# Performance work log

Hardware: AMD Instinct MI355X
Metric: run time of the kernel (lower is better)

Reference implementation:

```python
import jax, jax.numpy as jnp
import numpy as np

B, L, D = 8, 2048, 1024
NH = 16            # n_head
HD = D // NH       # 64; attention is (HD x HD) per token in this module


def setup_inputs() -> dict:
    key = jax.random.key(0)
    ks = jax.random.split(key, 5)
    s = 0.02  # init scale for weights
    return {
        "x": jax.random.normal(ks[0], (B, L, D), jnp.float32),
        "Wq": jax.random.normal(ks[1], (D, D), jnp.float32) * s,
        "bq": jnp.zeros((D,), jnp.float32),
        "Wk": jax.random.normal(ks[2], (D, D), jnp.float32) * s,
        "bk": jnp.zeros((D,), jnp.float32),
        "Wv": jax.random.normal(ks[3], (D, D), jnp.float32) * s,
        "bv": jnp.zeros((D,), jnp.float32),
        "Wo": jax.random.normal(ks[4], (D, D), jnp.float32) * s,
        "bo": jnp.zeros((D,), jnp.float32),
    }


def reference(x, Wq, bq, Wk, bk, Wv, bv, Wo, bo):
    b, l, d = x.shape
    # QKV projections
    q = (x @ Wq + bq).reshape(b, l, HD, NH)
    k = (x @ Wk + bk).reshape(b, l, HD, NH)
    v = (x @ Wv + bv).reshape(b, l, HD, NH)
    # NOTE: module reshapes to (b, l, head_dim, n_head), so scores are
    # per-token (HD, HD) with the NH axis contracted; norm = sqrt(NH).
    norm = jnp.sqrt(jnp.asarray(NH, x.dtype))
    attn = jnp.einsum('blij,blkj->blik', q, k) / norm  # (b, l, HD, HD)
    attn = attn + 1e-06
    # mask = tril of the VALUES; jnp.where uses nonzero-as-True semantics.
    mask = jnp.tril(attn)
    attn = jnp.where(mask, attn, -jnp.inf)
    probs = jax.nn.softmax(attn, axis=-1)
    y = jnp.einsum('blik,blkj->blij', probs, v).reshape(b, l, d)
    return y @ Wo + bo
```

## Files before the change

kernel.cpp:

```cpp
#include <hip/hip_runtime.h>
#include <hip/hip_bf16.h>
#include <stdint.h>

typedef unsigned short u16;

#define Bdim 8
#define Ldim 2048
#define Ddim 1024
#define NH 16
#define HD 64
#define MTOK (Bdim*Ldim)

#define BM 128
#define BN 128
#define BK 32

typedef __bf16 bf16x8 __attribute__((ext_vector_type(8)));
typedef float  f32x4  __attribute__((ext_vector_type(4)));
typedef float  f32x16 __attribute__((ext_vector_type(16)));

#define AS1 __attribute__((address_space(1)))
#define AS3 __attribute__((address_space(3)))

__device__ __forceinline__ void gload_lds16(const void* g, void* l) {
  __builtin_amdgcn_global_load_lds((const AS1 void*)g, (AS3 void*)l, 16, 0, 0);
}

__device__ __forceinline__ u16 f2bf(float f) {
  uint32_t u = __builtin_bit_cast(uint32_t, f);
  u += 0x7fffu + ((u >> 16) & 1u);
  return (u16)(u >> 16);
}
__device__ __forceinline__ uint32_t pkpair(float lo, float hi) {
  return (uint32_t)f2bf(lo) | ((uint32_t)f2bf(hi) << 16);
}

__global__ __launch_bounds__(256) void conv_f32_bf16(const float* __restrict__ in,
                                                     u16* __restrict__ out, int n4) {
  int i = blockIdx.x * 256 + threadIdx.x;
  if (i < n4) {
    float4 v = ((const float4*)in)[i];
    uint32_t w0 = (uint32_t)f2bf(v.x) | ((uint32_t)f2bf(v.y) << 16);
    uint32_t w1 = (uint32_t)f2bf(v.z) | ((uint32_t)f2bf(v.w) << 16);
    ((uint2*)out)[i] = make_uint2(w0, w1);
  }
}

__global__ __launch_bounds__(256) void conv_transpose_w(const float* __restrict__ W,
                                                        u16* __restrict__ Wt) {
  __shared__ float t[32][33];
  int tx = threadIdx.x & 31, ty = threadIdx.x >> 5;
  int k0 = blockIdx.x * 32, n0 = blockIdx.y * 32;
  #pragma unroll
  for (int i = 0; i < 32; i += 8)
    t[ty + i][tx] = W[(size_t)(k0 + ty + i) * Ddim + n0 + tx];
  __syncthreads();
  #pragma unroll
  for (int i = 0; i < 32; i += 8)
    Wt[(size_t)(n0 + ty + i) * Ddim + k0 + tx] = f2bf(t[tx][ty + i]);
}

template <int FUSED>
__global__ __launch_bounds__(256) void gemm_bt(const u16* __restrict__ A,
                                               const u16* __restrict__ Bt,
                                               const float* __restrict__ b0p,
                                               const float* __restrict__ b1p,
                                               const float* __restrict__ b2p,
                                               void* __restrict__ o0,
                                               void* __restrict__ o1,
                                               void* __restrict__ o2) {
  constexpr int K = 1024;
  __shared__ alignas(16) unsigned char pool[34816];
  u16* As = (u16*)pool;
  u16* Bs = As + 4096;
  const int tid = threadIdx.x;
  const int wid = tid >> 6, lane = tid & 63;
  const int bid = blockIdx.x;
  const int xcd = bid & 7, idx = bid >> 3;
  const int mt = (xcd << 4) | (idx & 15);
  const int nt = idx >> 4;
  const int m0 = mt * BM;
  const int n0g = nt * BN;
  const int wr = wid >> 1, wc = wid & 1;
  const int fr = lane & 15, fh = lane >> 4;

  f32x4 acc[4][4] = {};

  for (int k0 = 0; k0 < K; k0 += BK) {
    #pragma unroll
    for (int c = 0; c < 2; ++c) {
      int e = c * 2048 + wid * 512 + lane * 8;
      int r = e >> 5, col = e & 31;
      gload_lds16(A  + (size_t)(m0  + r) * K + (k0 + col), As + c * 2048 + wid * 512);
      gload_lds16(Bt + (size_t)(n0g + r) * K + (k0 + col), Bs + c * 2048 + wid * 512);
    }
    __syncthreads();

    bf16x8 af[4], bfr[4];
    #pragma unroll
    for (int m = 0; m < 4; ++m)
      af[m] = *(const bf16x8*)(As + (wr * 64 + m * 16 + fr) * BK + fh * 8);
    #pragma unroll
    for (int n = 0; n < 4; ++n)
      bfr[n] = *(const bf16x8*)(Bs + (wc * 64 + n * 16 + fr) * BK + fh * 8);
    #pragma unroll
    for (int m = 0; m < 4; ++m)
      #pragma unroll
      for (int n = 0; n < 4; ++n)
        acc[m][n] = __builtin_amdgcn_mfma_f32_16x16x32_bf16(af[m], bfr[n], acc[m][n], 0, 0, 0);
    __syncthreads();
  }

  if (FUSED) {
    const int which = nt >> 3;
    const int n0l = (nt & 7) * BN;
    const float* bias = which == 0 ? b0p : which == 1 ? b1p : b2p;
    u16* Out = (u16*)(which == 0 ? o0 : which == 1 ? o1 : o2);

    u16* Ct = (u16*)pool;
    #pragma unroll
    for (int n = 0; n < 4; ++n) {
      int col = wc * 64 + n * 16 + fr;
      float bvv = bias[n0l + col];
      #pragma unroll
      for (int m = 0; m < 4; ++m)
        #pragma unroll
        for (int r = 0; r < 4; ++r) {
          int row = wr * 64 + m * 16 + fh * 4 + r;
          Ct[row * 136 + col] = f2bf(acc[m][n][r] + bvv);
        }
    }
    __syncthreads();
    if (which != 2) {
      #pragma unroll
      for (int it = 0; it < 8; ++it) {
        int q = it * 256 + tid, r = q >> 4, cc = q & 15;
        uint4 v = *(const uint4*)(Ct + r * 136 + cc * 8);
        *(uint4*)(Out + (size_t)(m0 + r) * Ddim + n0l + cc * 8) = v;
      }
    } else {
      #pragma unroll
      for (int it = 0; it < 8; ++it) {
        int q = it * 256 + tid, r = q >> 4, i = q & 15;
        u16 tmp[8];
        #pragma unroll
        for (int j = 0; j < 8; ++j) tmp[j] = Ct[r * 136 + i + 16 * j];
        *(uint4*)(Out + (size_t)(m0 + r) * Ddim + i * 64 + (n0l >> 4)) = *(uint4*)tmp;
      }
    }
  } else {
    float* Cf = (float*)pool;
    float* Out = (float*)o0;
    #pragma unroll
    for (int h = 0; h < 2; ++h) {
      if (wc == h) {
        #pragma unroll
        for (int n = 0; n < 4; ++n) {
          int col = n * 16 + fr;
          float bvv = b0p[n0g + h * 64 + col];
          #pragma unroll
          for (int m = 0; m < 4; ++m)
            #pragma unroll
            for (int r = 0; r < 4; ++r) {
              int row = wr * 64 + m * 16 + fh * 4 + r;
              Cf[row * 68 + col] = acc[m][n][r] + bvv;
            }
        }
      }
      __syncthreads();
      #pragma unroll
      for (int it = 0; it < 8; ++it) {
        int q = it * 256 + tid, r = q >> 4, cc = q & 15;
        float4 v = *(const float4*)(Cf + r * 68 + cc * 4);
        *(float4*)(Out + (size_t)(m0 + r) * Ddim + n0g + h * 64 + cc * 4) = v;
      }
      __syncthreads();
    }
  }
}

__global__ __launch_bounds__(256) void attn_mfma(const u16* __restrict__ Q,
                                                 const u16* __restrict__ Kb,
                                                 const u16* __restrict__ Vt,
                                                 u16* __restrict__ Y) {
  const int wid = threadIdx.x >> 6, lane = threadIdx.x & 63;
  const int tok = blockIdx.x * 4 + wid;
  const size_t base = (size_t)tok * Ddim;
  const int hi = lane >> 5, c31 = lane & 31;

  const bf16x8 kf0 = *(const bf16x8*)(Kb + base + (size_t)c31 * NH + hi * 8);
  const bf16x8 kf1 = *(const bf16x8*)(Kb + base + (size_t)(32 + c31) * NH + hi * 8);
  const bf16x8 qf0 = *(const bf16x8*)(Q  + base + (size_t)c31 * NH + hi * 8);
  const bf16x8 qf1 = *(const bf16x8*)(Q  + base + (size_t)(32 + c31) * NH + hi * 8);
  bf16x8 bv[4];
  #pragma unroll
  for (int c = 0; c < 4; ++c)
    bv[c] = *(const bf16x8*)(Vt + base + (size_t)(lane & 15) * HD + c * 16 + hi * 8);

  const f32x16 z = {};
  f32x16 s00 = __builtin_amdgcn_mfma_f32_32x32x16_bf16(kf0, qf0, z, 0, 0, 0);
  f32x16 s01 = __builtin_amdgcn_mfma_f32_32x32x16_bf16(kf0, qf1, z, 0, 0, 0);
  f32x16 s11 = __builtin_amdgcn_mfma_f32_32x32x16_bf16(kf1, qf1, z, 0, 0, 0);

  float a[16], b0[16], b1[16];
  float mA = -3e38f, mB = -3e38f;
  #pragma unroll
  for (int r = 0; r < 16; ++r) {
    const int kl = (r & 3) + 8 * (r >> 2) + 4 * hi;
    const bool keep = kl <= c31;
    float v00 = fmaf(s00[r], 0.25f, 1e-6f);
    float v01 = fmaf(s01[r], 0.25f, 1e-6f);
    float v11 = fmaf(s11[r], 0.25f, 1e-6f);
    a[r]  = keep ? v00 : -3e38f;
    b0[r] = v01;
    b1[r] = keep ? v11 : -3e38f;
    mA = fmaxf(mA, a[r]);
    mB = fmaxf(mB, fmaxf(b0[r], b1[r]));
  }
  mA = fmaxf(mA, __shfl_xor(mA, 32, 64));
  mB = fmaxf(mB, __shfl_xor(mB, 32, 64));
  float sA = 0.f, sB = 0.f;
  #pragma unroll
  for (int r = 0; r < 16; ++r) {
    a[r]  = __expf(a[r]  - mA);  sA += a[r];
    b0[r] = __expf(b0[r] - mB);
    b1[r] = __expf(b1[r] - mB);  sB += b0[r] + b1[r];
  }
  sA += __shfl_xor(sA, 32, 64);
  sB += __shfl_xor(sB, 32, 64);
  const float iA = __builtin_amdgcn_rcpf(sA);
  const float iB = __builtin_amdgcn_rcpf(sB);

  uint32_t pA[4][2], pB0[4][2], pB1[4][2];
  #pragma unroll
  for (int m = 0; m < 4; ++m)
    #pragma unroll
    for (int t = 0; t < 2; ++t) {
      pA [m][t] = pkpair(a [4*m+2*t] * iA, a [4*m+2*t+1] * iA);
      pB0[m][t] = pkpair(b0[4*m+2*t] * iB, b0[4*m+2*t+1] * iB);
      pB1[m][t] = pkpair(b1[4*m+2*t] * iB, b1[4*m+2*t+1] * iB);
    }

#define AFRAG(dst, src, cp) do {                                              \
    uint32_t k0_ = hi ? src[2*(cp)+1][0] : src[2*(cp)][0];                    \
    uint32_t k1_ = hi ? src[2*(cp)+1][1] : src[2*(cp)][1];                    \
    uint32_t s0_ = hi ? src[2*(cp)][0]   : src[2*(cp)+1][0];                  \
    uint32_t s1_ = hi ? src[2*(cp)][1]   : src[2*(cp)+1][1];                  \
    uint32_t r0_ = (uint32_t)__shfl_xor((int)s0_, 32, 64);                    \
    uint32_t r1_ = (uint32_t)__shfl_xor((int)s1_, 32, 64);                    \
    union { uint32_t w[4]; bf16x8 v; } u_;                                    \
    u_.w[0] = hi ? r0_ : k0_;  u_.w[1] = hi ? r1_ : k1_;                      \
    u_.w[2] = hi ? k0_ : r0_;  u_.w[3] = hi ? k1_ : r1_;                      \
    dst = u_.v;                                                               \
  } while (0)

  f32x16 y0 = {}, y1 = {};
  bf16x8 af;
  AFRAG(af, pA, 0);  y0 = __builtin_amdgcn_mfma_f32_32x32x16_bf16(af, bv[0], y0, 0, 0, 0);
  AFRAG(af, pA, 1);  y0 = __builtin_amdgcn_mfma_f32_32x32x16_bf16(af, bv[1], y0, 0, 0, 0);
  AFRAG(af, pB0, 0); y1 = __builtin_amdgcn_mfma_f32_32x32x16_bf16(af, bv[0], y1, 0, 0, 0);
  AFRAG(af, pB0, 1); y1 = __builtin_amdgcn_mfma_f32_32x32x16_bf16(af, bv[1], y1, 0, 0, 0);
  AFRAG(af, pB1, 0); y1 = __builtin_amdgcn_mfma_f32_32x32x16_bf16(af, bv[2], y1, 0, 0, 0);
  AFRAG(af, pB1, 1); y1 = __builtin_amdgcn_mfma_f32_32x32x16_bf16(af, bv[3], y1, 0, 0, 0);
#undef AFRAG

  if (c31 < 16) {
    #pragma unroll
    for (int r = 0; r < 16; ++r) {
      const int row = (r & 3) + 8 * (r >> 2) + 4 * hi;
      Y[base + (size_t)row * NH + c31]        = f2bf(y0[r]);
      Y[base + (size_t)(32 + row) * NH + c31] = f2bf(y1[r]);
    }
  }
}

extern "C" void kernel_launch(void* const* d_in, const int* in_sizes, int n_in,
                              void* d_out, int out_size, void* d_ws, size_t ws_size,
                              hipStream_t stream) {
  const float* x  = (const float*)d_in[0];
  const float* Wq = (const float*)d_in[1];
  const float* bq = (const float*)d_in[2];
  const float* Wk = (const float*)d_in[3];
  const float* bk = (const float*)d_in[4];
  const float* Wv = (const float*)d_in[5];
  const float* bv = (const float*)d_in[6];
  const float* Wo = (const float*)d_in[7];
  const float* bo = (const float*)d_in[8];
  float* out = (float*)d_out;

  u16* xb = (u16*)d_ws;
  u16* Wt = xb + (size_t)MTOK * Ddim;
  u16* Qb = Wt + 4ull * Ddim * Ddim;
  u16* Kb = Qb + (size_t)MTOK * Ddim;
  u16* Vb = Kb + (size_t)MTOK * Ddim;
  u16* Yb = xb;

  conv_f32_bf16<<<(MTOK * Ddim / 4 + 255) / 256, 256, 0, stream>>>(x, xb, MTOK * Ddim / 4);

  dim3 tg(Ddim / 32, Ddim / 32);
  conv_transpose_w<<<tg, 256, 0, stream>>>(Wq, Wt + 0ull * Ddim * Ddim);
  conv_transpose_w<<<tg, 256, 0, stream>>>(Wk, Wt + 1ull * Ddim * Ddim);
  conv_transpose_w<<<tg, 256, 0, stream>>>(Wv, Wt + 2ull * Ddim * Ddim);
  conv_transpose_w<<<tg, 256, 0, stream>>>(Wo, Wt + 3ull * Ddim * Ddim);

  gemm_bt<1><<<dim3(3072), 256, 0, stream>>>(xb, Wt, bq, bk, bv, Qb, Kb, Vb);

  attn_mfma<<<MTOK / 4, 256, 0, stream>>>(Qb, Kb, Vb, Yb);

  gemm_bt<0><<<dim3(1024), 256, 0, stream>>>(Yb, Wt + 3ull * Ddim * Ddim,
                                             bo, bo, bo, out, out, out);
}
```

Measured before the change: 244.4 us.

## Rewrite projection GEMMs with 256x256 tiles, double-buffered LDS and swizzle

Both projection GEMMs move from 128x128 tiles with BK=32 and 256 threads to 256x256 tiles with BK=64 and 512 threads. Global-to-LDS loads are double-buffered so the next k-tile is prefetched while the current one is multiplied. LDS columns are XOR-swizzled to avoid bank conflicts, and MFMA priority is raised during compute. The goal is more operand reuse per load and latency hiding, at the cost of 128KB of LDS, more registers, fewer blocks (768 and 256) and an epilogue staged in halves or quarters.

Result: faster. 213.3 us (-12.7%).

```diff
diff --git a/kernel.cpp b/kernel.cpp
--- a/kernel.cpp
+++ b/kernel.cpp
@@ -10,10 +10,6 @@
 #define NH 16
 #define HD 64
 #define MTOK (Bdim*Ldim)
-
-#define BM 128
-#define BN 128
-#define BK 32
 
 typedef __bf16 bf16x8 __attribute__((ext_vector_type(8)));
 typedef float  f32x4  __attribute__((ext_vector_type(4)));
@@ -61,122 +57,167 @@
 }
 
 template <int FUSED>
-__global__ __launch_bounds__(256) void gemm_bt(const u16* __restrict__ A,
-                                               const u16* __restrict__ Bt,
-                                               const float* __restrict__ b0p,
-                                               const float* __restrict__ b1p,
-                                               const float* __restrict__ b2p,
-                                               void* __restrict__ o0,
-                                               void* __restrict__ o1,
-                                               void* __restrict__ o2) {
-  constexpr int K = 1024;
-  __shared__ alignas(16) unsigned char pool[34816];
-  u16* As = (u16*)pool;
-  u16* Bs = As + 4096;
+__global__ __launch_bounds__(512, 2) void gemm256(const u16* __restrict__ A,
+                                                  const u16* __restrict__ Bt,
+                                                  const float* __restrict__ b0p,
+                                                  const float* __restrict__ b1p,
+                                                  const float* __restrict__ b2p,
+                                                  void* __restrict__ o0,
+                                                  void* __restrict__ o1,
+                                                  void* __restrict__ o2) {
+  __shared__ alignas(16) u16 LP[65536];
+  u16* LA = LP;
+  u16* LB = LP + 32768;
+
   const int tid = threadIdx.x;
   const int wid = tid >> 6, lane = tid & 63;
+  const int wr = wid >> 2, wc = wid & 3;
+  const int fr = lane & 15, fh = lane >> 4;
+  const int key = fr & 7;
+
   const int bid = blockIdx.x;
   const int xcd = bid & 7, idx = bid >> 3;
-  const int mt = (xcd << 4) | (idx & 15);
-  const int nt = idx >> 4;
-  const int m0 = mt * BM;
-  const int n0g = nt * BN;
-  const int wr = wid >> 1, wc = wid & 1;
-  const int fr = lane & 15, fh = lane >> 4;
-
-  f32x4 acc[4][4] = {};
-
-  for (int k0 = 0; k0 < K; k0 += BK) {
-    #pragma unroll
-    for (int c = 0; c < 2; ++c) {
-      int e = c * 2048 + wid * 512 + lane * 8;
-      int r = e >> 5, col = e & 31;
-      gload_lds16(A  + (size_t)(m0  + r) * K + (k0 + col), As + c * 2048 + wid * 512);
-      gload_lds16(Bt + (size_t)(n0g + r) * K + (k0 + col), Bs + c * 2048 + wid * 512);
-    }
-    __syncthreads();
-
-    bf16x8 af[4], bfr[4];
-    #pragma unroll
-    for (int m = 0; m < 4; ++m)
-      af[m] = *(const bf16x8*)(As + (wr * 64 + m * 16 + fr) * BK + fh * 8);
-    #pragma unroll
-    for (int n = 0; n < 4; ++n)
-      bfr[n] = *(const bf16x8*)(Bs + (wc * 64 + n * 16 + fr) * BK + fh * 8);
-    #pragma unroll
-    for (int m = 0; m < 4; ++m)
-      #pragma unroll
-      for (int n = 0; n < 4; ++n)
-        acc[m][n] = __builtin_amdgcn_mfma_f32_16x16x32_bf16(af[m], bfr[n], acc[m][n], 0, 0, 0);
-    __syncthreads();
-  }
+  const int mt = xcd * 8 + (idx & 7);
+  const int nt = idx >> 3;
+  const int m0 = mt * 256;
+  const int n0g = nt * 256;
+
+  const int srow = wid * 8 + (lane >> 3);
+  const int scol = ((lane & 7) ^ (lane >> 3)) * 8;
+  const u16* aG = A  + (size_t)(m0  + srow) * 1024 + scol;
+  const u16* bG = Bt + (size_t)(n0g + srow) * 1024 + scol;
+  const int ldsW = wid * 512;
+
+#define STAGE(tile, buf) do {                                                  \
+    const u16* ag_ = aG + (size_t)(tile) * 64;                                  \
+    const u16* bg_ = bG + (size_t)(tile) * 64;                                  \
+    _Pragma("unroll")                                                           \
+    for (int s_ = 0; s_ < 4; ++s_) {                                            \
+      gload_lds16(ag_ + (size_t)s_ * 65536, LA + (buf) * 16384 + s_ * 4096 + ldsW); \
+      gload_lds16(bg_ + (size_t)s_ * 65536, LB + (buf) * 16384 + s_ * 4096 + ldsW); \
+    }                                                                           \
+  } while (0)
+
+  f32x4 acc[8][4] = {};
+
+#define COMPUTE(buf) do {                                                       \
+    _Pragma("unroll")                                                           \
+    for (int ks_ = 0; ks_ < 2; ++ks_) {                                         \
+      bf16x8 af_[8], bf_[4];                                                    \
+      const int p_ = ((ks_ * 4 + fh) ^ key) * 8;                                \
+      _Pragma("unroll")                                                         \
+      for (int m_ = 0; m_ < 8; ++m_)                                            \
+        af_[m_] = *(const bf16x8*)(LA + (buf) * 16384 +                         \
+                                   (wr * 128 + m_ * 16 + fr) * 64 + p_);        \
+      _Pragma("unroll")                                                         \
+      for (int n_ = 0; n_ < 4; ++n_)                                            \
+        bf_[n_] = *(const bf16x8*)(LB + (buf) * 16384 +                         \
+                                   (wc * 64 + n_ * 16 + fr) * 64 + p_);         \
+      __builtin_amdgcn_s_setprio(1);                                            \
+      _Pragma("unroll")                                                         \
+      for (int m_ = 0; m_ < 8; ++m_)                                            \
+        _Pragma("unroll")                                                       \
+        for (int n_ = 0; n_ < 4; ++n_)                                          \
+          acc[m_][n_] = __builtin_amdgcn_mfma_f32_16x16x32_bf16(                \
+              af_[m_], bf_[n_], acc[m_][n_], 0, 0, 0);                          \
+      __builtin_amdgcn_s_setprio(0);                                            \
+    }                                                                           \
+  } while (0)
+
+  STAGE(0, 0);
+  #pragma unroll 1
+  for (int t = 0; t < 15; ++t) {
+    const int cur = t & 1;
+    STAGE(t + 1, cur ^ 1);
+    asm volatile("s_waitcnt vmcnt(8)" ::: "memory");
+    __builtin_amdgcn_s_barrier();
+    COMPUTE(cur);
+    asm volatile("s_waitcnt lgkmcnt(0)" ::: "memory");
+    __builtin_amdgcn_s_barrier();
+  }
+  asm volatile("s_waitcnt vmcnt(0)" ::: "memory");
+  __builtin_amdgcn_s_barrier();
+  COMPUTE(1);
+  __syncthreads();
 
   if (FUSED) {
-    const int which = nt >> 3;
-    const int n0l = (nt & 7) * BN;
+    const int which = nt >> 2;
+    const int n0l = (nt & 3) * 256;
     const float* bias = which == 0 ? b0p : which == 1 ? b1p : b2p;
     u16* Out = (u16*)(which == 0 ? o0 : which == 1 ? o1 : o2);
-
-    u16* Ct = (u16*)pool;
-    #pragma unroll
-    for (int n = 0; n < 4; ++n) {
-      int col = wc * 64 + n * 16 + fr;
-      float bvv = bias[n0l + col];
-      #pragma unroll
-      for (int m = 0; m < 4; ++m)
+    u16* Ct = LP;
+    #pragma unroll 1
+    for (int h = 0; h < 2; ++h) {
+      if (h) __syncthreads();
+      if (wr == h) {
         #pragma unroll
-        for (int r = 0; r < 4; ++r) {
-          int row = wr * 64 + m * 16 + fh * 4 + r;
-          Ct[row * 136 + col] = f2bf(acc[m][n][r] + bvv);
+        for (int n = 0; n < 4; ++n) {
+          float bvv = bias[n0l + wc * 64 + n * 16 + fr];
+          #pragma unroll
+          for (int m = 0; m < 8; ++m)
+            #pragma unroll
+            for (int r = 0; r < 4; ++r)
+              Ct[wc * 9216 + (m * 16 + fh * 4 + r) * 72 + n * 16 + fr] =
+                  f2bf(acc[m][n][r] + bvv);
         }
-    }
-    __syncthreads();
-    if (which != 2) {
-      #pragma unroll
-      for (int it = 0; it < 8; ++it) {
-        int q = it * 256 + tid, r = q >> 4, cc = q & 15;
-        uint4 v = *(const uint4*)(Ct + r * 136 + cc * 8);
-        *(uint4*)(Out + (size_t)(m0 + r) * Ddim + n0l + cc * 8) = v;
       }
-    } else {
-      #pragma unroll
-      for (int it = 0; it < 8; ++it) {
-        int q = it * 256 + tid, r = q >> 4, i = q & 15;
-        u16 tmp[8];
+      __syncthreads();
+      if (which != 2) {
         #pragma unroll
-        for (int j = 0; j < 8; ++j) tmp[j] = Ct[r * 136 + i + 16 * j];
-        *(uint4*)(Out + (size_t)(m0 + r) * Ddim + i * 64 + (n0l >> 4)) = *(uint4*)tmp;
+        for (int j = 0; j < 8; ++j) {
+          int r = j * 16 + (tid >> 5), c8 = tid & 31;
+          uint4 v = *(const uint4*)(Ct + (c8 >> 3) * 9216 + r * 72 + (c8 & 7) * 8);
+          *(uint4*)(Out + (size_t)(m0 + h * 128 + r) * Ddim + n0l + c8 * 8) = v;
+        }
+      } else {
+        #pragma unroll
+        for (int j = 0; j < 4; ++j) {
+          int q = j * 512 + tid, r = q >> 4, i = q & 15;
+          u16 tmp[16];
+          #pragma unroll
+          for (int jj = 0; jj < 16; ++jj) {
+            int c = i + 16 * jj;
+            tmp[jj] = Ct[(c >> 6) * 9216 + r * 72 + (c & 63)];
+          }
+          u16* dst = Out + (size_t)(m0 + h * 128 + r) * Ddim + i * 64 + (n0l >> 4);
+          *(uint4*)dst = *(uint4*)tmp;
+          *(uint4*)(dst + 8) = *(uint4*)(tmp + 8);
+        }
       }
+      __syncthreads();
     }
   } else {
-    float* Cf = (float*)pool;
+    float* Cf = (float*)LP;
     float* Out = (float*)o0;
-    #pragma unroll
-    for (int h = 0; h < 2; ++h) {
-      if (wc == h) {
+    #pragma unroll 1
+    for (int h = 0; h < 4; ++h) {
+      if (h) __syncthreads();
+      if (wr == (h >> 1) && (wc >> 1) == (h & 1)) {
         #pragma unroll
         for (int n = 0; n < 4; ++n) {
-          int col = n * 16 + fr;
-          float bvv = b0p[n0g + h * 64 + col];
+          int col = (wc & 1) * 64 + n * 16 + fr;
+          float bvv = b0p[n0g + (h & 1) * 128 + col];
           #pragma unroll
-          for (int m = 0; m < 4; ++m)
+          for (int m = 0; m < 8; ++m)
             #pragma unroll
-            for (int r = 0; r < 4; ++r) {
-              int row = wr * 64 + m * 16 + fh * 4 + r;
-              Cf[row * 68 + col] = acc[m][n][r] + bvv;
-            }
+            for (int r = 0; r < 4; ++r)
+              Cf[(wc & 1) * 8704 + (m * 16 + fh * 4 + r) * 68 + n * 16 + fr] =
+                  acc[m][n][r] + bvv;
         }
       }
       __syncthreads();
       #pragma unroll
-      for (int it = 0; it < 8; ++it) {
-        int q = it * 256 + tid, r = q >> 4, cc = q & 15;
-        float4 v = *(const float4*)(Cf + r * 68 + cc * 4);
-        *(float4*)(Out + (size_t)(m0 + r) * Ddim + n0g + h * 64 + cc * 4) = v;
+      for (int j = 0; j < 8; ++j) {
+        int r = j * 16 + (tid >> 5), c4 = tid & 31;
+        float4 v = *(const float4*)(Cf + (c4 >> 4) * 8704 + r * 68 + (c4 & 15) * 4);
+        *(float4*)(Out + (size_t)(m0 + (h >> 1) * 128 + r) * Ddim +
+                   n0g + (h & 1) * 128 + c4 * 4) = v;
       }
       __syncthreads();
     }
   }
+#undef STAGE
+#undef COMPUTE
 }
 
 __global__ __launch_bounds__(256) void attn_mfma(const u16* __restrict__ Q,
@@ -303,10 +344,10 @@
   conv_transpose_w<<<tg, 256, 0, stream>>>(Wv, Wt + 2ull * Ddim * Ddim);
   conv_transpose_w<<<tg, 256, 0, stream>>>(Wo, Wt + 3ull * Ddim * Ddim);
 
-  gemm_bt<1><<<dim3(3072), 256, 0, stream>>>(xb, Wt, bq, bk, bv, Qb, Kb, Vb);
+  gemm256<1><<<dim3(768), 512, 0, stream>>>(xb, Wt, bq, bk, bv, Qb, Kb, Vb);
 
   attn_mfma<<<MTOK / 4, 256, 0, stream>>>(Qb, Kb, Vb, Yb);
 
-  gemm_bt<0><<<dim3(1024), 256, 0, stream>>>(Yb, Wt + 3ull * Ddim * Ddim,
-                                             bo, bo, bo, out, out, out);
-}
+  gemm256<0><<<dim3(256), 512, 0, stream>>>(Yb, Wt + 3ull * Ddim * Ddim,
+                                            bo, bo, bo, out, out, out);
+}
```

## Double-buffer GEMM with 128x256 tiles, 512 threads, and XOR-swizzled LDS

Applied to the files above, without the earlier changes.

Replaces the single-buffered 128x128 GEMM with a 128x256 tile per 512-thread block. The next K-slab's global-to-LDS loads are issued before computing the current one, using two LDS buffers, explicit vmcnt waits and raw barriers. LDS column chunks are XOR-swizzled to reduce bank conflicts, and s_setprio is raised around the MFMA burst. The epilogue is split into halves or quarters to fit LDS, which adds barriers, and the larger block with launch_bounds(512,4) adds register pressure.

Result: faster. 219.3 us (-10.3%).

```diff
diff --git a/kernel.cpp b/kernel.cpp
--- a/kernel.cpp
+++ b/kernel.cpp
@@ -10,10 +10,6 @@
 #define NH 16
 #define HD 64
 #define MTOK (Bdim*Ldim)
-
-#define BM 128
-#define BN 128
-#define BK 32
 
 typedef __bf16 bf16x8 __attribute__((ext_vector_type(8)));
 typedef float  f32x4  __attribute__((ext_vector_type(4)));
@@ -61,122 +57,155 @@
 }
 
 template <int FUSED>
-__global__ __launch_bounds__(256) void gemm_bt(const u16* __restrict__ A,
-                                               const u16* __restrict__ Bt,
-                                               const float* __restrict__ b0p,
-                                               const float* __restrict__ b1p,
-                                               const float* __restrict__ b2p,
-                                               void* __restrict__ o0,
-                                               void* __restrict__ o1,
-                                               void* __restrict__ o2) {
-  constexpr int K = 1024;
-  __shared__ alignas(16) unsigned char pool[34816];
-  u16* As = (u16*)pool;
-  u16* Bs = As + 4096;
+__global__ __launch_bounds__(512, 4) void gemmDP(const u16* __restrict__ A,
+                                                 const u16* __restrict__ Bt,
+                                                 const float* __restrict__ b0p,
+                                                 const float* __restrict__ b1p,
+                                                 const float* __restrict__ b2p,
+                                                 void* __restrict__ o0,
+                                                 void* __restrict__ o1,
+                                                 void* __restrict__ o2) {
+  __shared__ alignas(16) u16 LP[24576];
   const int tid = threadIdx.x;
   const int wid = tid >> 6, lane = tid & 63;
+  const int wr = wid >> 2, wc = wid & 3;
+  const int fr = lane & 15, fh = lane >> 4;
+  const int key = (fr >> 1) & 3;
+
   const int bid = blockIdx.x;
   const int xcd = bid & 7, idx = bid >> 3;
-  const int mt = (xcd << 4) | (idx & 15);
+  const int mt = xcd * 16 + (idx & 15);
   const int nt = idx >> 4;
-  const int m0 = mt * BM;
-  const int n0g = nt * BN;
-  const int wr = wid >> 1, wc = wid & 1;
-  const int fr = lane & 15, fh = lane >> 4;
+  const int m0 = mt * 128, n0g = nt * 256;
+
+  const int sr  = tid >> 2;
+  const int sgc = ((tid & 3) ^ ((tid >> 3) & 3)) * 8;
+  const u16* aS  = A  + (size_t)(m0 + sr)        * 1024 + sgc;
+  const u16* bS0 = Bt + (size_t)(n0g + sr)       * 1024 + sgc;
+  const u16* bS1 = Bt + (size_t)(n0g + 128 + sr) * 1024 + sgc;
+  const int ldA = wid * 512;
+
+#define STG(T, B_) do {                                                        \
+    gload_lds16(aS  + (T) * 32, LP + (B_) * 12288 + ldA);                      \
+    gload_lds16(bS0 + (T) * 32, LP + (B_) * 12288 + 4096 + ldA);               \
+    gload_lds16(bS1 + (T) * 32, LP + (B_) * 12288 + 8192 + ldA);               \
+  } while (0)
+
+#define WAITV(N) asm volatile("s_waitcnt vmcnt(" #N ")" ::: "memory")
+#define BAR() __builtin_amdgcn_s_barrier()
 
   f32x4 acc[4][4] = {};
 
-  for (int k0 = 0; k0 < K; k0 += BK) {
-    #pragma unroll
-    for (int c = 0; c < 2; ++c) {
-      int e = c * 2048 + wid * 512 + lane * 8;
-      int r = e >> 5, col = e & 31;
-      gload_lds16(A  + (size_t)(m0  + r) * K + (k0 + col), As + c * 2048 + wid * 512);
-      gload_lds16(Bt + (size_t)(n0g + r) * K + (k0 + col), Bs + c * 2048 + wid * 512);
-    }
-    __syncthreads();
-
-    bf16x8 af[4], bfr[4];
-    #pragma unroll
-    for (int m = 0; m < 4; ++m)
-      af[m] = *(const bf16x8*)(As + (wr * 64 + m * 16 + fr) * BK + fh * 8);
-    #pragma unroll
-    for (int n = 0; n < 4; ++n)
-      bfr[n] = *(const bf16x8*)(Bs + (wc * 64 + n * 16 + fr) * BK + fh * 8);
-    #pragma unroll
-    for (int m = 0; m < 4; ++m)
-      #pragma unroll
-      for (int n = 0; n < 4; ++n)
-        acc[m][n] = __builtin_amdgcn_mfma_f32_16x16x32_bf16(af[m], bfr[n], acc[m][n], 0, 0, 0);
-    __syncthreads();
-  }
+#define COMPUTE(B_) do {                                                       \
+    const u16* la_ = LP + (B_) * 12288;                                        \
+    const u16* lb_ = la_ + 4096;                                               \
+    const int p_ = (fh ^ key) * 8;                                             \
+    bf16x8 bf_[4];                                                             \
+    _Pragma("unroll")                                                          \
+    for (int n_ = 0; n_ < 4; ++n_)                                             \
+      bf_[n_] = *(const bf16x8*)(lb_ + (wc * 64 + n_ * 16 + fr) * 32 + p_);    \
+    __builtin_amdgcn_s_setprio(1);                                             \
+    _Pragma("unroll")                                                          \
+    for (int m_ = 0; m_ < 4; ++m_) {                                           \
+      bf16x8 am_ = *(const bf16x8*)(la_ + (wr * 64 + m_ * 16 + fr) * 32 + p_); \
+      _Pragma("unroll")                                                        \
+      for (int n_ = 0; n_ < 4; ++n_)                                           \
+        acc[m_][n_] = __builtin_amdgcn_mfma_f32_16x16x32_bf16(                 \
+            am_, bf_[n_], acc[m_][n_], 0, 0, 0);                               \
+    }                                                                          \
+    __builtin_amdgcn_s_setprio(0);                                             \
+  } while (0)
+
+  STG(0, 0);
+  #pragma unroll 1
+  for (int t = 0; t < 31; ++t) {
+    const int b = t & 1;
+    BAR();
+    STG(t + 1, b ^ 1);
+    WAITV(3);
+    BAR();
+    COMPUTE(b);
+  }
+  BAR();
+  WAITV(0);
+  BAR();
+  COMPUTE(1);
+  __syncthreads();
 
   if (FUSED) {
-    const int which = nt >> 3;
-    const int n0l = (nt & 7) * BN;
+    const int which = nt >> 2;
+    const int n0l = (nt & 3) * 256;
     const float* bias = which == 0 ? b0p : which == 1 ? b1p : b2p;
     u16* Out = (u16*)(which == 0 ? o0 : which == 1 ? o1 : o2);
-
-    u16* Ct = (u16*)pool;
-    #pragma unroll
-    for (int n = 0; n < 4; ++n) {
-      int col = wc * 64 + n * 16 + fr;
-      float bvv = bias[n0l + col];
-      #pragma unroll
-      for (int m = 0; m < 4; ++m)
+    u16* Ct = LP;
+    #pragma unroll 1
+    for (int h = 0; h < 2; ++h) {
+      if (h) __syncthreads();
+      if ((wc >> 1) == h) {
         #pragma unroll
-        for (int r = 0; r < 4; ++r) {
-          int row = wr * 64 + m * 16 + fh * 4 + r;
-          Ct[row * 136 + col] = f2bf(acc[m][n][r] + bvv);
+        for (int n = 0; n < 4; ++n) {
+          float bvv = bias[n0l + h * 128 + (wc & 1) * 64 + n * 16 + fr];
+          #pragma unroll
+          for (int m = 0; m < 4; ++m)
+            #pragma unroll
+            for (int r = 0; r < 4; ++r)
+              Ct[(wr * 64 + m * 16 + fh * 4 + r) * 136 +
+                 (wc & 1) * 64 + n * 16 + fr] = f2bf(acc[m][n][r] + bvv);
         }
-    }
-    __syncthreads();
-    if (which != 2) {
-      #pragma unroll
-      for (int it = 0; it < 8; ++it) {
-        int q = it * 256 + tid, r = q >> 4, cc = q & 15;
-        uint4 v = *(const uint4*)(Ct + r * 136 + cc * 8);
-        *(uint4*)(Out + (size_t)(m0 + r) * Ddim + n0l + cc * 8) = v;
       }
-    } else {
-      #pragma unroll
-      for (int it = 0; it < 8; ++it) {
-        int q = it * 256 + tid, r = q >> 4, i = q & 15;
-        u16 tmp[8];
+      __syncthreads();
+      if (which != 2) {
         #pragma unroll
-        for (int j = 0; j < 8; ++j) tmp[j] = Ct[r * 136 + i + 16 * j];
-        *(uint4*)(Out + (size_t)(m0 + r) * Ddim + i * 64 + (n0l >> 4)) = *(uint4*)tmp;
+        for (int j = 0; j < 4; ++j) {
+          int unit = j * 512 + tid, row = unit >> 4, c8 = unit & 15;
+          uint4 v = *(const uint4*)(Ct + row * 136 + c8 * 8);
+          *(uint4*)(Out + (size_t)(m0 + row) * Ddim + n0l + h * 128 + c8 * 8) = v;
+        }
+      } else {
+        #pragma unroll
+        for (int j = 0; j < 4; ++j) {
+          int unit = j * 512 + tid, row = unit >> 4, i = unit & 15;
+          u16 tmp[8];
+          #pragma unroll
+          for (int jj = 0; jj < 8; ++jj) tmp[jj] = Ct[row * 136 + i + 16 * jj];
+          *(uint4*)(Out + (size_t)(m0 + row) * Ddim + i * 64 +
+                    (n0l >> 4) + h * 8) = *(uint4*)tmp;
+        }
       }
+      __syncthreads();
     }
   } else {
-    float* Cf = (float*)pool;
+    float* Cf = (float*)LP;
     float* Out = (float*)o0;
-    #pragma unroll
-    for (int h = 0; h < 2; ++h) {
+    #pragma unroll 1
+    for (int h = 0; h < 4; ++h) {
+      if (h) __syncthreads();
       if (wc == h) {
         #pragma unroll
         for (int n = 0; n < 4; ++n) {
-          int col = n * 16 + fr;
-          float bvv = b0p[n0g + h * 64 + col];
+          float bvv = b0p[n0g + h * 64 + n * 16 + fr];
           #pragma unroll
           for (int m = 0; m < 4; ++m)
             #pragma unroll
-            for (int r = 0; r < 4; ++r) {
-              int row = wr * 64 + m * 16 + fh * 4 + r;
-              Cf[row * 68 + col] = acc[m][n][r] + bvv;
-            }
+            for (int r = 0; r < 4; ++r)
+              Cf[(wr * 64 + m * 16 + fh * 4 + r) * 68 + n * 16 + fr] =
+                  acc[m][n][r] + bvv;
         }
       }
       __syncthreads();
       #pragma unroll
-      for (int it = 0; it < 8; ++it) {
-        int q = it * 256 + tid, r = q >> 4, cc = q & 15;
-        float4 v = *(const float4*)(Cf + r * 68 + cc * 4);
-        *(float4*)(Out + (size_t)(m0 + r) * Ddim + n0g + h * 64 + cc * 4) = v;
+      for (int j = 0; j < 4; ++j) {
+        int unit = j * 512 + tid, row = unit >> 4, c4 = unit & 15;
+        float4 v = *(const float4*)(Cf + row * 68 + c4 * 4);
+        *(float4*)(Out + (size_t)(m0 + row) * Ddim + n0g + h * 64 + c4 * 4) = v;
       }
       __syncthreads();
     }
   }
+#undef STG
+#undef WAITV
+#undef BAR
+#undef COMPUTE
 }
 
 __global__ __launch_bounds__(256) void attn_mfma(const u16* __restrict__ Q,
@@ -303,10 +332,10 @@
   conv_transpose_w<<<tg, 256, 0, stream>>>(Wv, Wt + 2ull * Ddim * Ddim);
   conv_transpose_w<<<tg, 256, 0, stream>>>(Wo, Wt + 3ull * Ddim * Ddim);
 
-  gemm_bt<1><<<dim3(3072), 256, 0, stream>>>(xb, Wt, bq, bk, bv, Qb, Kb, Vb);
+  gemmDP<1><<<dim3(1536), 512, 0, stream>>>(xb, Wt, bq, bk, bv, Qb, Kb, Vb);
 
   attn_mfma<<<MTOK / 4, 256, 0, stream>>>(Qb, Kb, Vb, Yb);
 
-  gemm_bt<0><<<dim3(1024), 256, 0, stream>>>(Yb, Wt + 3ull * Ddim * Ddim,
-                                             bo, bo, bo, out, out, out);
-}
+  gemmDP<0><<<dim3(512), 512, 0, stream>>>(Yb, Wt + 3ull * Ddim * Ddim,
+                                           bo, bo, bo, out, out, out);
+}
```
